# Optimization experiments

Hardware: AMD Instinct MI355X
Metric: run time of the kernel (lower is better)

## Reference

```python
import jax, jax.numpy as jnp
import numpy as np
from jax import lax

FEAT_DIM = 4096
OUT_DIM = 512
T = 2048


def setup_inputs() -> dict:
    key = jax.random.key(0)
    k1, k2, k3 = jax.random.split(key, 3)
    x = jax.random.normal(k1, (FEAT_DIM, T), dtype=jnp.float32)
    # reservoir pushforward weights (_gen_weights is abstract; use scaled gaussian
    # so the clamped recurrence stays well-conditioned, spectral radius ~0.9)
    W_res = jax.random.normal(k2, (FEAT_DIM, FEAT_DIM), dtype=jnp.float32) * (0.9 / np.sqrt(FEAT_DIM))
    # readout, matching `0.1 * torch.randn(out_dim, feat_dim)`
    w_out = 0.1 * jax.random.normal(k3, (OUT_DIM, FEAT_DIM), dtype=jnp.float32)
    return {"x": x, "W_res": W_res, "w_out": w_out}


def reference(x, W_res, w_out):
    # x: [feat_dim, T]; W_res: [feat_dim, feat_dim]; w_out: [out_dim, feat_dim]
    # Recurrence: feats_{t} = clamp(W_res @ feats_{t-1} + x_t, -1, 1)
    #             out_t    = w_out @ feats_t
    n_feat = W_res.shape[0]

    def step(feats, x_t):
        feats = jnp.clip(W_res @ feats + x_t, -1.0, 1.0)
        return feats, w_out @ feats

    feats0 = jnp.zeros((n_feat,), dtype=x.dtype)
    _, outs = lax.scan(step, feats0, x.T)  # outs: [T, out_dim]
    return outs.T  # [out_dim, T]
```

## Files before the change

### kernel.cpp

```cpp
#include <hip/hip_runtime.h>

#define F     4096
#define T     2048
#define NBLK  256
#define NTHR  1024
#define K     4


typedef unsigned long long u64;
typedef unsigned int u32;
typedef unsigned short u16;

template <int CTRL>
__device__ __forceinline__ float dpp_add(float x) {
    int xi = __builtin_bit_cast(int, x);
    int yi = __builtin_amdgcn_update_dpp(0, xi, CTRL, 0xf, 0xf, false);
    return x + __builtin_bit_cast(float, yi);
}

__device__ __forceinline__ float wave_sum(float x) {
    x = dpp_add<0x111>(x);
    x = dpp_add<0x112>(x);
    x = dpp_add<0x114>(x);
    x = dpp_add<0x118>(x);
    x = dpp_add<0x142>(x);
    x = dpp_add<0x143>(x);
    return x;
}

#define PIN4(v) asm volatile("" : "+v"((v).x), "+v"((v).y), "+v"((v).z), "+v"((v).w))

__device__ __forceinline__ u64 cload_u64(const u64* p) {
    return __hip_atomic_load(p, __ATOMIC_RELAXED, __HIP_MEMORY_SCOPE_AGENT);
}
__device__ __forceinline__ void cstore_u32(u32* p, u32 v) {
    __hip_atomic_store(p, v, __ATOMIC_RELAXED, __HIP_MEMORY_SCOPE_AGENT);
}

__device__ __forceinline__ float half_to_f(u32 bits) {
    return (float)__builtin_bit_cast(_Float16, (u16)(bits & 0xffffu));
}

__global__ __launch_bounds__(NTHR, 4) void rc_kernel(
    const float* __restrict__ x, const float* __restrict__ Wres,
    const float* __restrict__ wout, float* __restrict__ out,
    u32* __restrict__ ring)
{
    __shared__ __align__(16) float fl[F];
    __shared__ float red[2][16][4];
    __shared__ float redo[2][16];

    const int tid  = threadIdx.x;
    const int b    = blockIdx.x;
    const int w    = tid >> 6;
    const int lane = tid & 63;
    const int wr   = w & 3;
    const int wk   = w >> 2;

    const int row0 = b * 16 + wr * 4;
    const int kofs = wk * 1024 + lane * 4;
    float4 wreg[4][4];
#pragma unroll
    for (int j = 0; j < 4; ++j) {
        const float* wp = Wres + (size_t)(row0 + j) * F + kofs;
#pragma unroll
        for (int i = 0; i < 4; ++i)
            wreg[j][i] = *(const float4*)(wp + i * 256);
    }
#pragma unroll
    for (int j = 0; j < 4; ++j) {
        PIN4(wreg[j][0]); PIN4(wreg[j][1]); PIN4(wreg[j][2]); PIN4(wreg[j][3]);
    }

    const int rrow = b * 2 + (wr & 1);
    const int i0   = (wr >> 1) * 2;
    const float* wop = wout + (size_t)rrow * F + kofs + i0 * 256;
    float4 wo0 = *(const float4*)(wop);
    float4 wo1 = *(const float4*)(wop + 256);
    PIN4(wo0); PIN4(wo1);

    float xval = 0.f;
    if (tid < 16) xval = x[(size_t)(b * 16 + tid) * T + 0];

    const int ep = w * 256 + lane * 4;

    for (int t = 0; t <= T; ++t) {
        if (t > 0) {
            const u32* rs = ring + (size_t)((t - 1) & (K - 1)) * F + ep;
            const u32 tag = (u32)t;
            u64 p01 = cload_u64((const u64*)rs);
            u64 p23 = cload_u64((const u64*)(rs + 2));
            bool okA = ((u32)(p01 & 0xffffffffu) >> 16 == tag)
                     & ((u32)(p01 >> 32) >> 16 == tag);
            bool okB = ((u32)(p23 & 0xffffffffu) >> 16 == tag)
                     & ((u32)(p23 >> 32) >> 16 == tag);
            while (!__all(okA & okB)) {
                __builtin_amdgcn_s_sleep(1);
                if (!okA) {
                    p01 = cload_u64((const u64*)rs);
                    okA = ((u32)(p01 & 0xffffffffu) >> 16 == tag)
                        & ((u32)(p01 >> 32) >> 16 == tag);
                }
                if (!okB) {
                    p23 = cload_u64((const u64*)(rs + 2));
                    okB = ((u32)(p23 & 0xffffffffu) >> 16 == tag)
                        & ((u32)(p23 >> 32) >> 16 == tag);
                }
            }
            float4 v;
            v.x = half_to_f((u32)(p01 & 0xffffffffu));
            v.y = half_to_f((u32)(p01 >> 32));
            v.z = half_to_f((u32)(p23 & 0xffffffffu));
            v.w = half_to_f((u32)(p23 >> 32));
            *(float4*)&fl[ep] = v;
        } else {
            *(float4*)&fl[ep] = make_float4(0.f, 0.f, 0.f, 0.f);
        }
        __syncthreads();

        float4 f0 = *(const float4*)&fl[kofs + 0 * 256];
        float4 f1 = *(const float4*)&fl[kofs + 1 * 256];
        float4 f2 = *(const float4*)&fl[kofs + 2 * 256];
        float4 f3 = *(const float4*)&fl[kofs + 3 * 256];

        float acc0 = 0.f, acc1 = 0.f, acc2 = 0.f, acc3 = 0.f;
#define DOT_STEP(i, fv) \
        acc0 += wreg[0][i].x * fv.x + wreg[0][i].y * fv.y + wreg[0][i].z * fv.z + wreg[0][i].w * fv.w; \
        acc1 += wreg[1][i].x * fv.x + wreg[1][i].y * fv.y + wreg[1][i].z * fv.z + wreg[1][i].w * fv.w; \
        acc2 += wreg[2][i].x * fv.x + wreg[2][i].y * fv.y + wreg[2][i].z * fv.z + wreg[2][i].w * fv.w; \
        acc3 += wreg[3][i].x * fv.x + wreg[3][i].y * fv.y + wreg[3][i].z * fv.z + wreg[3][i].w * fv.w;
        DOT_STEP(0, f0)
        DOT_STEP(1, f1)
        DOT_STEP(2, f2)
        DOT_STEP(3, f3)
#undef DOT_STEP

        float4 ra, rb;
        if (i0 == 0) { ra = f0; rb = f1; } else { ra = f2; rb = f3; }
        float p = wo0.x * ra.x + wo0.y * ra.y + wo0.z * ra.z + wo0.w * ra.w
                + wo1.x * rb.x + wo1.y * rb.y + wo1.z * rb.z + wo1.w * rb.w;

        acc0 = wave_sum(acc0);
        acc1 = wave_sum(acc1);
        acc2 = wave_sum(acc2);
        acc3 = wave_sum(acc3);
        p    = wave_sum(p);
        const int pb = t & 1;
        if (lane == 63) {
            red[pb][w][0] = acc0; red[pb][w][1] = acc1;
            red[pb][w][2] = acc2; red[pb][w][3] = acc3;
            redo[pb][w] = p;
        }
        __syncthreads();

        if (w == 0 && t < T) {
            if (lane < 16) {
                const int r = lane, rw = r >> 2, rj = r & 3;
                float s = red[pb][rw][rj] + red[pb][rw + 4][rj]
                        + red[pb][rw + 8][rj] + red[pb][rw + 12][rj];
                s += xval;
                s = fminf(1.f, fmaxf(-1.f, s));
                u32 hb = (u32)__builtin_bit_cast(u16, (_Float16)s);
                u32 pk = ((u32)(t + 1) << 16) | hb;
                cstore_u32(ring + (size_t)(t & (K - 1)) * F + b * 16 + r, pk);
                const int tn = (t + 1 < T) ? (t + 1) : (T - 1);
                xval = x[(size_t)(b * 16 + lane) * T + tn];
            }
        }

        if (t > 0 && tid >= 64 && tid < 66) {
            const int r = tid - 64;
            float s = redo[pb][r]      + redo[pb][r + 2]  + redo[pb][r + 4]
                    + redo[pb][r + 6]  + redo[pb][r + 8]  + redo[pb][r + 10]
                    + redo[pb][r + 12] + redo[pb][r + 14];
            out[(size_t)(b * 2 + r) * T + (t - 1)] = s;
        }
    }
}

extern "C" void kernel_launch(void* const* d_in, const int* in_sizes, int n_in,
                              void* d_out, int out_size, void* d_ws, size_t ws_size,
                              hipStream_t stream) {
    const float* x    = (const float*)d_in[0];
    const float* Wres = (const float*)d_in[1];
    const float* wout = (const float*)d_in[2];
    float* out        = (float*)d_out;
    u32* ring         = (u32*)((char*)d_ws + 4096);


    void* args[] = { (void*)&x, (void*)&Wres, (void*)&wout, (void*)&out,
                     (void*)&ring };
    (void)hipLaunchCooperativeKernel((const void*)rc_kernel, dim3(NBLK), dim3(NTHR),
                                     args, 0, stream);
}
```

Measured before the change: 6.954 ms.

## Replace second block barrier with LDS fixed-point atomic reductions and double-buffered features

Removes the second __syncthreads per timestep. Each wave now folds its partial row sums into a shared 64-bit counter+value word using fixed-point atomic adds, and the last arriving wave finalizes the clamp and publishes to the ring. The feature buffer is double-buffered by step parity so one barrier per step is enough. This trades some float precision for the fixed-point encoding, and the spin-poll loop is simplified to reload both halves together.

```diff
diff --git a/kernel.cpp b/kernel.cpp
--- a/kernel.cpp
+++ b/kernel.cpp
@@ -41,14 +41,15 @@
     return (float)__builtin_bit_cast(_Float16, (u16)(bits & 0xffffu));
 }
 
+
 __global__ __launch_bounds__(NTHR, 4) void rc_kernel(
     const float* __restrict__ x, const float* __restrict__ Wres,
     const float* __restrict__ wout, float* __restrict__ out,
     u32* __restrict__ ring)
 {
-    __shared__ __align__(16) float fl[F];
-    __shared__ float red[2][16][4];
-    __shared__ float redo[2][16];
+    __shared__ __align__(16) float fl[2][F];
+    __shared__ u64 accf[2][16];
+    __shared__ u64 acco[2][2];
 
     const int tid  = threadIdx.x;
     const int b    = blockIdx.x;
@@ -56,6 +57,9 @@
     const int lane = tid & 63;
     const int wr   = w & 3;
     const int wk   = w >> 2;
+
+    if (tid < 32) accf[tid >> 4][tid & 15] = 0ull;
+    if (tid < 4)  acco[tid >> 1][tid & 1]  = 0ull;
 
     const int row0 = b * 16 + wr * 4;
     const int kofs = wk * 1024 + lane * 4;
@@ -79,49 +83,52 @@
     float4 wo1 = *(const float4*)(wop + 256);
     PIN4(wo0); PIN4(wo1);
 
-    float xval = 0.f;
-    if (tid < 16) xval = x[(size_t)(b * 16 + tid) * T + 0];
+    const int g    = lane >> 4;
+    const bool pub = (lane & 15) == 15;
+
+    float xv = 0.f;
+    if (pub) xv = x[(size_t)(row0 + g) * T + 0];
+
+    __syncthreads();
 
     const int ep = w * 256 + lane * 4;
 
     for (int t = 0; t <= T; ++t) {
+        const int par = t & 1;
+
         if (t > 0) {
             const u32* rs = ring + (size_t)((t - 1) & (K - 1)) * F + ep;
             const u32 tag = (u32)t;
             u64 p01 = cload_u64((const u64*)rs);
             u64 p23 = cload_u64((const u64*)(rs + 2));
-            bool okA = ((u32)(p01 & 0xffffffffu) >> 16 == tag)
-                     & ((u32)(p01 >> 32) >> 16 == tag);
-            bool okB = ((u32)(p23 & 0xffffffffu) >> 16 == tag)
-                     & ((u32)(p23 >> 32) >> 16 == tag);
-            while (!__all(okA & okB)) {
+            bool ok = ((u32)(p01 & 0xffffffffu) >> 16 == tag)
+                    & ((u32)(p01 >> 32) >> 16 == tag)
+                    & ((u32)(p23 & 0xffffffffu) >> 16 == tag)
+                    & ((u32)(p23 >> 32) >> 16 == tag);
+            while (!__all(ok)) {
                 __builtin_amdgcn_s_sleep(1);
-                if (!okA) {
-                    p01 = cload_u64((const u64*)rs);
-                    okA = ((u32)(p01 & 0xffffffffu) >> 16 == tag)
-                        & ((u32)(p01 >> 32) >> 16 == tag);
-                }
-                if (!okB) {
-                    p23 = cload_u64((const u64*)(rs + 2));
-                    okB = ((u32)(p23 & 0xffffffffu) >> 16 == tag)
-                        & ((u32)(p23 >> 32) >> 16 == tag);
-                }
+                p01 = cload_u64((const u64*)rs);
+                p23 = cload_u64((const u64*)(rs + 2));
+                ok = ((u32)(p01 & 0xffffffffu) >> 16 == tag)
+                   & ((u32)(p01 >> 32) >> 16 == tag)
+                   & ((u32)(p23 & 0xffffffffu) >> 16 == tag)
+                   & ((u32)(p23 >> 32) >> 16 == tag);
             }
             float4 v;
             v.x = half_to_f((u32)(p01 & 0xffffffffu));
             v.y = half_to_f((u32)(p01 >> 32));
             v.z = half_to_f((u32)(p23 & 0xffffffffu));
             v.w = half_to_f((u32)(p23 >> 32));
-            *(float4*)&fl[ep] = v;
+            *(float4*)&fl[par][ep] = v;
         } else {
-            *(float4*)&fl[ep] = make_float4(0.f, 0.f, 0.f, 0.f);
+            *(float4*)&fl[par][ep] = make_float4(0.f, 0.f, 0.f, 0.f);
         }
         __syncthreads();
 
-        float4 f0 = *(const float4*)&fl[kofs + 0 * 256];
-        float4 f1 = *(const float4*)&fl[kofs + 1 * 256];
-        float4 f2 = *(const float4*)&fl[kofs + 2 * 256];
-        float4 f3 = *(const float4*)&fl[kofs + 3 * 256];
+        float4 f0 = *(const float4*)&fl[par][kofs + 0 * 256];
+        float4 f1 = *(const float4*)&fl[par][kofs + 1 * 256];
+        float4 f2 = *(const float4*)&fl[par][kofs + 2 * 256];
+        float4 f3 = *(const float4*)&fl[par][kofs + 3 * 256];
 
         float acc0 = 0.f, acc1 = 0.f, acc2 = 0.f, acc3 = 0.f;
 #define DOT_STEP(i, fv) \
@@ -145,35 +152,40 @@
         acc2 = wave_sum(acc2);
         acc3 = wave_sum(acc3);
         p    = wave_sum(p);
-        const int pb = t & 1;
-        if (lane == 63) {
-            red[pb][w][0] = acc0; red[pb][w][1] = acc1;
-            red[pb][w][2] = acc2; red[pb][w][3] = acc3;
-            redo[pb][w] = p;
-        }
-        __syncthreads();
-
-        if (w == 0 && t < T) {
-            if (lane < 16) {
-                const int r = lane, rw = r >> 2, rj = r & 3;
-                float s = red[pb][rw][rj] + red[pb][rw + 4][rj]
-                        + red[pb][rw + 8][rj] + red[pb][rw + 12][rj];
-                s += xval;
+
+        float r0 = __shfl(acc0, 63), r1 = __shfl(acc1, 63),
+              r2 = __shfl(acc2, 63), r3 = __shfl(acc3, 63);
+        float myrow = (g == 0) ? r0 : (g == 1) ? r1 : (g == 2) ? r2 : r3;
+
+        if (pub && t < T) {
+            u32 biased = (u32)(__float2int_rn(myrow * 16777216.f) + 0x20000000);
+            u64 c = (1ull << 32) | (u64)biased;
+            u64 old = atomicAdd(&accf[par][wr * 4 + g], c);
+            if ((u32)(old >> 32) == 3u) {
+                u32 tot = (u32)old + biased;
+                int fx  = (int)(tot ^ 0x80000000u);
+                float s = (float)fx * (1.f / 16777216.f) + xv;
                 s = fminf(1.f, fmaxf(-1.f, s));
                 u32 hb = (u32)__builtin_bit_cast(u16, (_Float16)s);
-                u32 pk = ((u32)(t + 1) << 16) | hb;
-                cstore_u32(ring + (size_t)(t & (K - 1)) * F + b * 16 + r, pk);
-                const int tn = (t + 1 < T) ? (t + 1) : (T - 1);
-                xval = x[(size_t)(b * 16 + lane) * T + tn];
+                accf[par][wr * 4 + g] = 0ull;
+                cstore_u32(ring + (size_t)(t & (K - 1)) * F + b * 16 + wr * 4 + g,
+                           ((u32)(t + 1) << 16) | hb);
             }
+            const int tn = (t + 1 < T) ? (t + 1) : (T - 1);
+            xv = x[(size_t)(row0 + g) * T + tn];
         }
 
-        if (t > 0 && tid >= 64 && tid < 66) {
-            const int r = tid - 64;
-            float s = redo[pb][r]      + redo[pb][r + 2]  + redo[pb][r + 4]
-                    + redo[pb][r + 6]  + redo[pb][r + 8]  + redo[pb][r + 10]
-                    + redo[pb][r + 12] + redo[pb][r + 14];
-            out[(size_t)(b * 2 + r) * T + (t - 1)] = s;
+        if (lane == 63 && t > 0) {
+            u32 biased = (u32)(__float2int_rn(p * 4194304.f) + 0x10000000);
+            u64 c = (1ull << 32) | (u64)biased;
+            const int r = wr & 1;
+            u64 old = atomicAdd(&acco[par][r], c);
+            if ((u32)(old >> 32) == 7u) {
+                u32 tot = (u32)old + biased;
+                int fx  = (int)(tot ^ 0x80000000u);
+                acco[par][r] = 0ull;
+                out[(size_t)(b * 2 + r) * T + (t - 1)] = (float)fx * (1.f / 4194304.f);
+            }
         }
     }
 }
```

Result: slower. 9.091 ms (+30.7%).

## Replace block barriers with tagged LDS flags for intra-block dataflow

Applied to the files above, without the earlier changes.

Removes both __syncthreads per timestep. Ring values are copied into a double-buffered LDS array together with their step tags, and partial sums are written to LDS with tags. Each wave spins on the tags of just the LDS chunks it needs and consumes them as they arrive, and wave 0 spins on the partial-sum tags. The goal is to cut barrier latency on the serial critical path of the recurrence. The cost is LDS spin-polling and relaxed workgroup-scope atomics, which may have memory-ordering subtleties.

```diff
diff --git a/kernel.cpp b/kernel.cpp
--- a/kernel.cpp
+++ b/kernel.cpp
@@ -36,6 +36,12 @@
 __device__ __forceinline__ void cstore_u32(u32* p, u32 v) {
     __hip_atomic_store(p, v, __ATOMIC_RELAXED, __HIP_MEMORY_SCOPE_AGENT);
 }
+__device__ __forceinline__ u64 lds_load64(const u64* p) {
+    return __hip_atomic_load(p, __ATOMIC_RELAXED, __HIP_MEMORY_SCOPE_WORKGROUP);
+}
+__device__ __forceinline__ void lds_store64(u64* p, u64 v) {
+    __hip_atomic_store(p, v, __ATOMIC_RELAXED, __HIP_MEMORY_SCOPE_WORKGROUP);
+}
 
 __device__ __forceinline__ float half_to_f(u32 bits) {
     return (float)__builtin_bit_cast(_Float16, (u16)(bits & 0xffffu));
@@ -46,9 +52,9 @@
     const float* __restrict__ wout, float* __restrict__ out,
     u32* __restrict__ ring)
 {
-    __shared__ __align__(16) float fl[F];
-    __shared__ float red[2][16][4];
-    __shared__ float redo[2][16];
+    __shared__ __align__(16) u32 fl[2][F];
+    __shared__ u64 redp[2][64];
+    __shared__ u64 redo[2][16];
 
     const int tid  = threadIdx.x;
     const int b    = blockIdx.x;
@@ -56,6 +62,12 @@
     const int lane = tid & 63;
     const int wr   = w & 3;
     const int wk   = w >> 2;
+    const int g    = lane >> 4;
+
+#pragma unroll
+    for (int i = 0; i < 8; ++i) ((u32*)fl)[tid + i * NTHR] = 0xFFFF0000u;
+    if (tid < 128) ((u64*)redp)[tid] = 0ull;
+    if (tid < 32)  ((u64*)redo)[tid] = 0ull;
 
     const int row0 = b * 16 + wr * 4;
     const int kofs = wk * 1024 + lane * 4;
@@ -79,101 +91,135 @@
     float4 wo1 = *(const float4*)(wop + 256);
     PIN4(wo0); PIN4(wo1);
 
-    float xval = 0.f;
-    if (tid < 16) xval = x[(size_t)(b * 16 + tid) * T + 0];
+    __syncthreads();
+
+    float xv = 0.f;
+    if (w == 0 && (lane & 3) == 0) xv = x[(size_t)(b * 16 + (lane >> 2)) * T + 0];
 
     const int ep = w * 256 + lane * 4;
 
     for (int t = 0; t <= T; ++t) {
+        const int par = t & 1;
+        const u32 ctag = (u32)t;
+
         if (t > 0) {
             const u32* rs = ring + (size_t)((t - 1) & (K - 1)) * F + ep;
-            const u32 tag = (u32)t;
-            u64 p01 = cload_u64((const u64*)rs);
-            u64 p23 = cload_u64((const u64*)(rs + 2));
-            bool okA = ((u32)(p01 & 0xffffffffu) >> 16 == tag)
-                     & ((u32)(p01 >> 32) >> 16 == tag);
-            bool okB = ((u32)(p23 & 0xffffffffu) >> 16 == tag)
-                     & ((u32)(p23 >> 32) >> 16 == tag);
-            while (!__all(okA & okB)) {
+            bool done = false;
+            for (;;) {
+                if (!done) {
+                    u64 p01 = cload_u64((const u64*)rs);
+                    u64 p23 = cload_u64((const u64*)(rs + 2));
+                    bool ok = ((u32)p01 >> 16 == ctag) & ((u32)(p01 >> 32) >> 16 == ctag)
+                            & ((u32)p23 >> 16 == ctag) & ((u32)(p23 >> 32) >> 16 == ctag);
+                    if (ok) {
+                        lds_store64((u64*)&fl[par][ep], p01);
+                        lds_store64((u64*)&fl[par][ep + 2], p23);
+                        done = true;
+                    }
+                }
+                if (__all(done)) break;
                 __builtin_amdgcn_s_sleep(1);
-                if (!okA) {
-                    p01 = cload_u64((const u64*)rs);
-                    okA = ((u32)(p01 & 0xffffffffu) >> 16 == tag)
-                        & ((u32)(p01 >> 32) >> 16 == tag);
-                }
-                if (!okB) {
-                    p23 = cload_u64((const u64*)(rs + 2));
-                    okB = ((u32)(p23 & 0xffffffffu) >> 16 == tag)
-                        & ((u32)(p23 >> 32) >> 16 == tag);
-                }
             }
-            float4 v;
-            v.x = half_to_f((u32)(p01 & 0xffffffffu));
-            v.y = half_to_f((u32)(p01 >> 32));
-            v.z = half_to_f((u32)(p23 & 0xffffffffu));
-            v.w = half_to_f((u32)(p23 >> 32));
-            *(float4*)&fl[ep] = v;
         } else {
-            *(float4*)&fl[ep] = make_float4(0.f, 0.f, 0.f, 0.f);
-        }
-        __syncthreads();
-
-        float4 f0 = *(const float4*)&fl[kofs + 0 * 256];
-        float4 f1 = *(const float4*)&fl[kofs + 1 * 256];
-        float4 f2 = *(const float4*)&fl[kofs + 2 * 256];
-        float4 f3 = *(const float4*)&fl[kofs + 3 * 256];
-
-        float acc0 = 0.f, acc1 = 0.f, acc2 = 0.f, acc3 = 0.f;
-#define DOT_STEP(i, fv) \
-        acc0 += wreg[0][i].x * fv.x + wreg[0][i].y * fv.y + wreg[0][i].z * fv.z + wreg[0][i].w * fv.w; \
-        acc1 += wreg[1][i].x * fv.x + wreg[1][i].y * fv.y + wreg[1][i].z * fv.z + wreg[1][i].w * fv.w; \
-        acc2 += wreg[2][i].x * fv.x + wreg[2][i].y * fv.y + wreg[2][i].z * fv.z + wreg[2][i].w * fv.w; \
-        acc3 += wreg[3][i].x * fv.x + wreg[3][i].y * fv.y + wreg[3][i].z * fv.z + wreg[3][i].w * fv.w;
-        DOT_STEP(0, f0)
-        DOT_STEP(1, f1)
-        DOT_STEP(2, f2)
-        DOT_STEP(3, f3)
-#undef DOT_STEP
-
-        float4 ra, rb;
-        if (i0 == 0) { ra = f0; rb = f1; } else { ra = f2; rb = f3; }
-        float p = wo0.x * ra.x + wo0.y * ra.y + wo0.z * ra.z + wo0.w * ra.w
-                + wo1.x * rb.x + wo1.y * rb.y + wo1.z * rb.z + wo1.w * rb.w;
+            lds_store64((u64*)&fl[0][ep], 0ull);
+            lds_store64((u64*)&fl[0][ep + 2], 0ull);
+        }
+
+        float acc0 = 0.f, acc1 = 0.f, acc2 = 0.f, acc3 = 0.f, p = 0.f;
+        u32 pend = 0xFu;
+        while (pend) {
+#pragma unroll
+            for (int i = 0; i < 4; ++i) {
+                if (pend & (1u << i)) {
+                    const u64* ap = (const u64*)&fl[par][kofs + i * 256];
+                    u64 a  = lds_load64(ap);
+                    u64 c2 = lds_load64(ap + 1);
+                    bool ok = ((u32)a  >> 16 == ctag) & ((u32)(a  >> 32) >> 16 == ctag)
+                            & ((u32)c2 >> 16 == ctag) & ((u32)(c2 >> 32) >> 16 == ctag);
+                    if (__all(ok)) {
+                        float4 f;
+                        f.x = half_to_f((u32)a);  f.y = half_to_f((u32)(a  >> 32));
+                        f.z = half_to_f((u32)c2); f.w = half_to_f((u32)(c2 >> 32));
+                        acc0 += wreg[0][i].x * f.x + wreg[0][i].y * f.y + wreg[0][i].z * f.z + wreg[0][i].w * f.w;
+                        acc1 += wreg[1][i].x * f.x + wreg[1][i].y * f.y + wreg[1][i].z * f.z + wreg[1][i].w * f.w;
+                        acc2 += wreg[2][i].x * f.x + wreg[2][i].y * f.y + wreg[2][i].z * f.z + wreg[2][i].w * f.w;
+                        acc3 += wreg[3][i].x * f.x + wreg[3][i].y * f.y + wreg[3][i].z * f.z + wreg[3][i].w * f.w;
+                        if (i == i0)
+                            p += wo0.x * f.x + wo0.y * f.y + wo0.z * f.z + wo0.w * f.w;
+                        else if (i == i0 + 1)
+                            p += wo1.x * f.x + wo1.y * f.y + wo1.z * f.z + wo1.w * f.w;
+                        pend &= ~(1u << i);
+                    }
+                }
+            }
+        }
 
         acc0 = wave_sum(acc0);
         acc1 = wave_sum(acc1);
         acc2 = wave_sum(acc2);
         acc3 = wave_sum(acc3);
         p    = wave_sum(p);
-        const int pb = t & 1;
+
+        float r0 = __shfl(acc0, 63), r1 = __shfl(acc1, 63),
+              r2 = __shfl(acc2, 63), r3 = __shfl(acc3, 63);
+        const u32 rt = (u32)(t + 1);
+        if ((lane & 15) == 15) {
+            float myrow = (g == 0) ? r0 : (g == 1) ? r1 : (g == 2) ? r2 : r3;
+            lds_store64(&redp[par][(wr * 4 + g) * 4 + wk],
+                        ((u64)rt << 32) | (u64)__builtin_bit_cast(u32, myrow));
+        }
         if (lane == 63) {
-            red[pb][w][0] = acc0; red[pb][w][1] = acc1;
-            red[pb][w][2] = acc2; red[pb][w][3] = acc3;
-            redo[pb][w] = p;
-        }
-        __syncthreads();
-
-        if (w == 0 && t < T) {
-            if (lane < 16) {
-                const int r = lane, rw = r >> 2, rj = r & 3;
-                float s = red[pb][rw][rj] + red[pb][rw + 4][rj]
-                        + red[pb][rw + 8][rj] + red[pb][rw + 12][rj];
-                s += xval;
-                s = fminf(1.f, fmaxf(-1.f, s));
-                u32 hb = (u32)__builtin_bit_cast(u16, (_Float16)s);
-                u32 pk = ((u32)(t + 1) << 16) | hb;
-                cstore_u32(ring + (size_t)(t & (K - 1)) * F + b * 16 + r, pk);
-                const int tn = (t + 1 < T) ? (t + 1) : (T - 1);
-                xval = x[(size_t)(b * 16 + lane) * T + tn];
+            lds_store64(&redo[par][(wr & 1) * 8 + wk * 2 + (wr >> 1)],
+                        ((u64)rt << 32) | (u64)__builtin_bit_cast(u32, p));
+        }
+
+        if (w == 0) {
+            if (t < T) {
+                u64 q, q2 = 0;
+                for (;;) {
+                    q = lds_load64(&redp[par][lane]);
+                    bool ok = ((u32)(q >> 32) == rt);
+                    if (lane < 16) {
+                        q2 = lds_load64(&redo[par][lane]);
+                        ok &= ((u32)(q2 >> 32) == rt);
+                    }
+                    if (__all(ok)) break;
+                }
+                float v = __builtin_bit_cast(float, (u32)q);
+                v += __shfl_xor(v, 1);
+                v += __shfl_xor(v, 2);
+                if ((lane & 3) == 0) {
+                    float s = v + xv;
+                    s = fminf(1.f, fmaxf(-1.f, s));
+                    u32 hb = (u32)__builtin_bit_cast(u16, (_Float16)s);
+                    cstore_u32(ring + (size_t)(t & (K - 1)) * F + b * 16 + (lane >> 2),
+                               (rt << 16) | hb);
+                    const int tn = (t + 1 < T) ? (t + 1) : (T - 1);
+                    xv = x[(size_t)(b * 16 + (lane >> 2)) * T + tn];
+                }
+                if (t > 0 && lane < 16) {
+                    float rv = __builtin_bit_cast(float, (u32)q2);
+                    rv += __shfl_xor(rv, 1);
+                    rv += __shfl_xor(rv, 2);
+                    rv += __shfl_xor(rv, 4);
+                    if ((lane & 7) == 0)
+                        out[(size_t)(b * 2 + (lane >> 3)) * T + (t - 1)] = rv;
+                }
+            } else {
+                if (lane < 16) {
+                    u64 q2;
+                    for (;;) {
+                        q2 = lds_load64(&redo[par][lane]);
+                        if (__all((u32)(q2 >> 32) == rt)) break;
+                    }
+                    float rv = __builtin_bit_cast(float, (u32)q2);
+                    rv += __shfl_xor(rv, 1);
+                    rv += __shfl_xor(rv, 2);
+                    rv += __shfl_xor(rv, 4);
+                    if ((lane & 7) == 0)
+                        out[(size_t)(b * 2 + (lane >> 3)) * T + (T - 1)] = rv;
+                }
             }
-        }
-
-        if (t > 0 && tid >= 64 && tid < 66) {
-            const int r = tid - 64;
-            float s = redo[pb][r]      + redo[pb][r + 2]  + redo[pb][r + 4]
-                    + redo[pb][r + 6]  + redo[pb][r + 8]  + redo[pb][r + 10]
-                    + redo[pb][r + 12] + redo[pb][r + 14];
-            out[(size_t)(b * 2 + r) * T + (t - 1)] = s;
         }
     }
 }
```

Result: slower. 8.053 ms (+15.8%).

## Replace second block barrier with tagged shared-memory partials and spin-wait

Applied to the files above, without the earlier changes.

Each wave writes its partial sums into shared memory packed with a step tag, and the barrier after the reduction is removed. Wave 0 spins on the tags for the 16 reservoir rows, finishes the sum, clamps and publishes to the ring at raised priority. Wave 1 separately spins on the readout partials and reduces them with shuffles. The aim is to take a full-block barrier off the serial critical path of every time step, at the cost of spin polling on volatile shared memory and a double-buffer reuse that now depends on the remaining barrier for safety.

```diff
diff --git a/kernel.cpp b/kernel.cpp
--- a/kernel.cpp
+++ b/kernel.cpp
@@ -41,14 +41,18 @@
     return (float)__builtin_bit_cast(_Float16, (u16)(bits & 0xffffu));
 }
 
+__device__ __forceinline__ u64 pack_tf(u32 tag, float v) {
+    return ((u64)tag << 32) | (u64)__builtin_bit_cast(u32, v);
+}
+
 __global__ __launch_bounds__(NTHR, 4) void rc_kernel(
     const float* __restrict__ x, const float* __restrict__ Wres,
     const float* __restrict__ wout, float* __restrict__ out,
     u32* __restrict__ ring)
 {
     __shared__ __align__(16) float fl[F];
-    __shared__ float red[2][16][4];
-    __shared__ float redo[2][16];
+    __shared__ volatile u64 redq[2][16][5];
+    __shared__ volatile u64 redqo[2][16];
 
     const int tid  = threadIdx.x;
     const int b    = blockIdx.x;
@@ -56,6 +60,9 @@
     const int lane = tid & 63;
     const int wr   = w & 3;
     const int wk   = w >> 2;
+
+    if (tid < 160) ((u64*)redq)[tid]  = 0ull;
+    if (tid < 32)  ((u64*)redqo)[tid] = 0ull;
 
     const int row0 = b * 16 + wr * 4;
     const int kofs = wk * 1024 + lane * 4;
@@ -82,9 +89,14 @@
     float xval = 0.f;
     if (tid < 16) xval = x[(size_t)(b * 16 + tid) * T + 0];
 
+    __syncthreads();
+
     const int ep = w * 256 + lane * 4;
 
     for (int t = 0; t <= T; ++t) {
+        const int pb  = t & 1;
+        const u32 rt  = (u32)(t + 1);
+
         if (t > 0) {
             const u32* rs = ring + (size_t)((t - 1) & (K - 1)) * F + ep;
             const u32 tag = (u32)t;
@@ -145,36 +157,55 @@
         acc2 = wave_sum(acc2);
         acc3 = wave_sum(acc3);
         p    = wave_sum(p);
-        const int pb = t & 1;
         if (lane == 63) {
-            red[pb][w][0] = acc0; red[pb][w][1] = acc1;
-            red[pb][w][2] = acc2; red[pb][w][3] = acc3;
-            redo[pb][w] = p;
-        }
-        __syncthreads();
+            redq[pb][wr * 4 + 0][wk] = pack_tf(rt, acc0);
+            redq[pb][wr * 4 + 1][wk] = pack_tf(rt, acc1);
+            redq[pb][wr * 4 + 2][wk] = pack_tf(rt, acc2);
+            redq[pb][wr * 4 + 3][wk] = pack_tf(rt, acc3);
+            redqo[pb][w] = pack_tf(rt, p);
+        }
 
         if (w == 0 && t < T) {
+            __builtin_amdgcn_s_setprio(1);
+            const int rr = lane & 15;
+            u64 q0, q1, q2, q3; bool ok;
+            do {
+                q0 = redq[pb][rr][0]; q1 = redq[pb][rr][1];
+                q2 = redq[pb][rr][2]; q3 = redq[pb][rr][3];
+                ok = ((u32)(q0 >> 32) == rt) & ((u32)(q1 >> 32) == rt)
+                   & ((u32)(q2 >> 32) == rt) & ((u32)(q3 >> 32) == rt);
+            } while (!__all(ok));
+            float s = (__builtin_bit_cast(float, (u32)q0) + __builtin_bit_cast(float, (u32)q1))
+                    + (__builtin_bit_cast(float, (u32)q2) + __builtin_bit_cast(float, (u32)q3))
+                    + xval;
+            s = fminf(1.f, fmaxf(-1.f, s));
+            u32 hb = (u32)__builtin_bit_cast(u16, (_Float16)s);
             if (lane < 16) {
-                const int r = lane, rw = r >> 2, rj = r & 3;
-                float s = red[pb][rw][rj] + red[pb][rw + 4][rj]
-                        + red[pb][rw + 8][rj] + red[pb][rw + 12][rj];
-                s += xval;
-                s = fminf(1.f, fmaxf(-1.f, s));
-                u32 hb = (u32)__builtin_bit_cast(u16, (_Float16)s);
-                u32 pk = ((u32)(t + 1) << 16) | hb;
-                cstore_u32(ring + (size_t)(t & (K - 1)) * F + b * 16 + r, pk);
+                cstore_u32(ring + (size_t)(t & (K - 1)) * F + b * 16 + lane,
+                           (rt << 16) | hb);
+            }
+            __builtin_amdgcn_s_setprio(0);
+            if (lane < 16) {
                 const int tn = (t + 1 < T) ? (t + 1) : (T - 1);
                 xval = x[(size_t)(b * 16 + lane) * T + tn];
             }
         }
 
-        if (t > 0 && tid >= 64 && tid < 66) {
-            const int r = tid - 64;
-            float s = redo[pb][r]      + redo[pb][r + 2]  + redo[pb][r + 4]
-                    + redo[pb][r + 6]  + redo[pb][r + 8]  + redo[pb][r + 10]
-                    + redo[pb][r + 12] + redo[pb][r + 14];
-            out[(size_t)(b * 2 + r) * T + (t - 1)] = s;
-        }
+        if (w == 1 && t > 0) {
+            const int rr = lane & 15;
+            u64 q; bool ok;
+            do {
+                q = redqo[pb][rr];
+                ok = ((u32)(q >> 32) == rt);
+            } while (!__all(ok));
+            float v = __builtin_bit_cast(float, (u32)q);
+            v += __shfl_xor(v, 2);
+            v += __shfl_xor(v, 4);
+            v += __shfl_xor(v, 8);
+            if (lane < 2)
+                out[(size_t)(b * 2 + lane) * T + (t - 1)] = v;
+        }
+
     }
 }
 
```

New measurement: 7.899 ms. 1.14x slower.
